# Performance work log

Hardware: AMD Instinct MI355X
Metric: run time of the kernel (lower is better)

Reference implementation:

```python
import jax, jax.numpy as jnp
import numpy as np

N_NODES = 512
IN_FEATURES = 512
N_HEADS = 8
N_HIDDEN = 64  # out_features // n_heads
NEG_SLOPE = 0.2


def setup_inputs() -> dict:
    key = jax.random.key(0)
    k_h, k_ws, k_wt, k_a, k_adj = jax.random.split(key, 5)
    lim_w = 1.0 / np.sqrt(IN_FEATURES)
    lim_a = 1.0 / np.sqrt(N_HIDDEN)
    h = jax.random.normal(k_h, (1, N_NODES, IN_FEATURES), dtype=jnp.float32)
    # nn.Linear weights: [out, in]
    W_source = jax.random.uniform(k_ws, (N_HEADS * N_HIDDEN, IN_FEATURES), jnp.float32, -lim_w, lim_w)
    W_target = jax.random.uniform(k_wt, (N_HEADS * N_HIDDEN, IN_FEATURES), jnp.float32, -lim_w, lim_w)
    attn_w = jax.random.uniform(k_a, (N_HIDDEN,), jnp.float32, -lim_a, lim_a)  # Linear(n_hidden, 1)
    adjacency_matrix = jax.random.randint(k_adj, (N_NODES, N_NODES, 1), 0, 2, dtype=jnp.int32)
    return {"h": h, "W_source": W_source, "W_target": W_target,
            "attn_w": attn_w, "adjacency_matrix": adjacency_matrix}


def reference(h, W_source, W_target, attn_w, adjacency_matrix):
    n_nodes = h.shape[1]
    x = h[0]  # [N, D]; module assumes batch == 1
    g_source = (x @ W_source.T).reshape(n_nodes, N_HEADS, N_HIDDEN)  # [N,H,F]
    g_target = (x @ W_target.T).reshape(n_nodes, N_HEADS, N_HIDDEN)  # [N,H,F]
    # g_sum[i, j] = g_source[j] + g_target[i]  (repeat / repeat_interleave semantics)
    g_sum = g_source[None, :, :, :] + g_target[:, None, :, :]  # [N,N,H,F]
    act = jnp.where(g_sum >= 0, g_sum, NEG_SLOPE * g_sum)       # LeakyReLU
    scores = jnp.einsum('ijhf,f->ijh', act, attn_w)              # [N,N,H]
    scores = jnp.where(adjacency_matrix == 0, -jnp.inf, scores)  # adj broadcasts over heads
    attention = jax.nn.softmax(scores, axis=1)                   # softmax over source nodes j
    # dropout p applied at eval -> identity
    head_output = jnp.einsum('ijh,jhf->ihf', attention, g_target)  # [N,H,F]
    out = head_output.reshape(n_nodes, N_HEADS * N_HIDDEN)         # is_concat=True
    return out, attention
```

## Files before the change

### kernel.cpp

```cpp
#include <hip/hip_runtime.h>
#include <hip/hip_bf16.h>

#define NN 512
#define IND 512
#define NH 8
#define NF 64
#define NEG_SLOPE 0.2f

__global__ __launch_bounds__(256) void gemm_xwT(
    const float* __restrict__ X,
    const float* __restrict__ Ws,
    const float* __restrict__ Wt,
    float* __restrict__ Gs, float* __restrict__ Gt)
{
    const float* W = (blockIdx.z == 0) ? Ws : Wt;
    float* C = (blockIdx.z == 0) ? Gs : Gt;

    __shared__ float As[32][33];
    __shared__ float Bs[32][33];

    const int tid = threadIdx.x;
    const int n0 = blockIdx.y * 32;
    const int o0 = blockIdx.x * 32;
    const int row = tid >> 3;
    const int kg  = (tid & 7) * 4;
    const int ty = tid >> 4;
    const int tx = tid & 15;

    float c00 = 0.f, c01 = 0.f, c10 = 0.f, c11 = 0.f;

    for (int kt = 0; kt < IND; kt += 32) {
        float4 pa = *reinterpret_cast<const float4*>(X + (size_t)(n0 + row) * IND + kt + kg);
        As[row][kg + 0] = pa.x;
        As[row][kg + 1] = pa.y;
        As[row][kg + 2] = pa.z;
        As[row][kg + 3] = pa.w;
        float4 pb = *reinterpret_cast<const float4*>(W + (size_t)(o0 + row) * IND + kt + kg);
        Bs[row][kg + 0] = pb.x;
        Bs[row][kg + 1] = pb.y;
        Bs[row][kg + 2] = pb.z;
        Bs[row][kg + 3] = pb.w;
        __syncthreads();
        #pragma unroll
        for (int k = 0; k < 32; ++k) {
            float a0 = As[ty][k], a1 = As[ty + 16][k];
            float b0 = Bs[tx][k], b1 = Bs[tx + 16][k];
            c00 += a0 * b0; c01 += a0 * b1;
            c10 += a1 * b0; c11 += a1 * b1;
        }
        __syncthreads();
    }
    C[(size_t)(n0 + ty) * IND + o0 + tx]            = c00;
    C[(size_t)(n0 + ty) * IND + o0 + tx + 16]       = c01;
    C[(size_t)(n0 + ty + 16) * IND + o0 + tx]       = c10;
    C[(size_t)(n0 + ty + 16) * IND + o0 + tx + 16]  = c11;
}

__global__ __launch_bounds__(256) void gat_attn(
    const float* __restrict__ Gs, const float* __restrict__ Gt,
    const float* __restrict__ attn_w,
    const int* __restrict__ adj,
    float* __restrict__ out_feat,
    float* __restrict__ out_att)
{
    __shared__ float s_gt[4][64];
    __shared__ float s_w[64];
    __shared__ float s_sc[4][512];
    __shared__ float s_red[4][4][64];

    const int tid = threadIdx.x;
    const int i0 = blockIdx.x * 4;
    const int h  = blockIdx.y;

    {
        int ii = tid >> 6, f = tid & 63;
        s_gt[ii][f] = Gt[(size_t)(i0 + ii) * IND + h * NF + f];
        if (tid < 64) s_w[tid] = attn_w[tid];
    }
    __syncthreads();

    #pragma unroll
    for (int rep = 0; rep < 2; ++rep) {
        int j = tid + rep * 256;
        float a0 = 0.f, a1 = 0.f, a2 = 0.f, a3 = 0.f;
        const float4* gp = reinterpret_cast<const float4*>(Gs + (size_t)j * IND + h * NF);
        #pragma unroll 4
        for (int f4 = 0; f4 < 16; ++f4) {
            float4 g = gp[f4];
            #pragma unroll
            for (int c = 0; c < 4; ++c) {
                float gv = (c == 0) ? g.x : (c == 1) ? g.y : (c == 2) ? g.z : g.w;
                int f = f4 * 4 + c;
                float w = s_w[f];
                float t;
                t = gv + s_gt[0][f]; t = (t >= 0.f) ? t : NEG_SLOPE * t; a0 += t * w;
                t = gv + s_gt[1][f]; t = (t >= 0.f) ? t : NEG_SLOPE * t; a1 += t * w;
                t = gv + s_gt[2][f]; t = (t >= 0.f) ? t : NEG_SLOPE * t; a2 += t * w;
                t = gv + s_gt[3][f]; t = (t >= 0.f) ? t : NEG_SLOPE * t; a3 += t * w;
            }
        }
        s_sc[0][j] = adj[(size_t)(i0 + 0) * NN + j] ? a0 : -INFINITY;
        s_sc[1][j] = adj[(size_t)(i0 + 1) * NN + j] ? a1 : -INFINITY;
        s_sc[2][j] = adj[(size_t)(i0 + 2) * NN + j] ? a2 : -INFINITY;
        s_sc[3][j] = adj[(size_t)(i0 + 3) * NN + j] ? a3 : -INFINITY;
    }
    __syncthreads();

    {
        const int wave = tid >> 6, lane = tid & 63;
        const int ii = wave;
        float m = -INFINITY;
        #pragma unroll
        for (int r = 0; r < 8; ++r) m = fmaxf(m, s_sc[ii][lane + r * 64]);
        #pragma unroll
        for (int off = 32; off >= 1; off >>= 1) m = fmaxf(m, __shfl_xor(m, off, 64));
        float e[8];
        float sum = 0.f;
        #pragma unroll
        for (int r = 0; r < 8; ++r) {
            float v = s_sc[ii][lane + r * 64];
            float ev = __expf(v - m);
            e[r] = ev;
            sum += ev;
        }
        #pragma unroll
        for (int off = 32; off >= 1; off >>= 1) sum += __shfl_xor(sum, off, 64);
        float inv = 1.f / sum;
        int i = i0 + ii;
        #pragma unroll
        for (int r = 0; r < 8; ++r) {
            int j = lane + r * 64;
            float a = e[r] * inv;
            s_sc[ii][j] = a;
            out_att[((size_t)i * NN + j) * NH + h] = a;
        }
    }
    __syncthreads();

    {
        const int f = tid & 63, q = tid >> 6;
        float a0 = 0.f, a1 = 0.f, a2 = 0.f, a3 = 0.f;
        for (int j = q * 128; j < q * 128 + 128; ++j) {
            float gv = Gt[(size_t)j * IND + h * NF + f];
            a0 += s_sc[0][j] * gv;
            a1 += s_sc[1][j] * gv;
            a2 += s_sc[2][j] * gv;
            a3 += s_sc[3][j] * gv;
        }
        s_red[q][0][f] = a0; s_red[q][1][f] = a1;
        s_red[q][2][f] = a2; s_red[q][3][f] = a3;
    }
    __syncthreads();
    {
        int ii = tid >> 6, f = tid & 63;
        float s = s_red[0][ii][f] + s_red[1][ii][f] + s_red[2][ii][f] + s_red[3][ii][f];
        out_feat[(size_t)(i0 + ii) * (NH * NF) + h * NF + f] = s;
    }
}

extern "C" void kernel_launch(void* const* d_in, const int* in_sizes, int n_in,
                              void* d_out, int out_size, void* d_ws, size_t ws_size,
                              hipStream_t stream) {
    const float* X  = (const float*)d_in[0];
    const float* Ws = (const float*)d_in[1];
    const float* Wt = (const float*)d_in[2];
    const float* aw = (const float*)d_in[3];
    const int* adj  = (const int*)d_in[4];

    float* Gs = (float*)d_ws;
    float* Gt = Gs + (size_t)NN * IND;

    float* out_feat = (float*)d_out;
    float* out_att  = out_feat + (size_t)NN * NH * NF;

    hipLaunchKernelGGL(gemm_xwT, dim3(16, 16, 2), dim3(256), 0, stream,
                       X, Ws, Wt, Gs, Gt);
    hipLaunchKernelGGL(gat_attn, dim3(NN / 4, NH), dim3(256), 0, stream,
                       Gs, Gt, aw, adj, out_feat, out_att);
}
```

Measured before the change: 120.9 us.

## Transpose inputs, compute Gs transposed via new GEMM, rework attention score loop

Adds a transpose kernel for X and W_target, then replaces the shared-memory tiled GEMM with a register-accumulating GEMM that splits K across waves. This GEMM writes Gs in a [feature, node] layout so the score loop reads contiguous float2 across nodes. LeakyReLU is rewritten as 0.6x+0.4|x| fused into FMAs, and the aggregation loop reads attention weights as float4 from shared memory. It adds an extra kernel launch and more workspace traffic for the transposes.

New measurement: 108.6 us. 1.11x faster.

```diff
diff --git a/kernel.cpp b/kernel.cpp
--- a/kernel.cpp
+++ b/kernel.cpp
@@ -1,114 +1,144 @@
 #include <hip/hip_runtime.h>
-#include <hip/hip_bf16.h>
 
 #define NN 512
 #define IND 512
 #define NH 8
 #define NF 64
-#define NEG_SLOPE 0.2f
-
-__global__ __launch_bounds__(256) void gemm_xwT(
-    const float* __restrict__ X,
-    const float* __restrict__ Ws,
-    const float* __restrict__ Wt,
-    float* __restrict__ Gs, float* __restrict__ Gt)
+
+__global__ __launch_bounds__(256) void transpose512(
+    const float* __restrict__ X, float* __restrict__ Xt,
+    const float* __restrict__ Wtg, float* __restrict__ Wtg_t)
 {
-    const float* W = (blockIdx.z == 0) ? Ws : Wt;
-    float* C = (blockIdx.z == 0) ? Gs : Gt;
-
-    __shared__ float As[32][33];
-    __shared__ float Bs[32][33];
-
+    const float* src = blockIdx.z ? Wtg : X;
+    float* dst       = blockIdx.z ? Wtg_t : Xt;
+    __shared__ float tile[32][33];
     const int tid = threadIdx.x;
-    const int n0 = blockIdx.y * 32;
-    const int o0 = blockIdx.x * 32;
-    const int row = tid >> 3;
-    const int kg  = (tid & 7) * 4;
-    const int ty = tid >> 4;
-    const int tx = tid & 15;
-
-    float c00 = 0.f, c01 = 0.f, c10 = 0.f, c11 = 0.f;
-
-    for (int kt = 0; kt < IND; kt += 32) {
-        float4 pa = *reinterpret_cast<const float4*>(X + (size_t)(n0 + row) * IND + kt + kg);
-        As[row][kg + 0] = pa.x;
-        As[row][kg + 1] = pa.y;
-        As[row][kg + 2] = pa.z;
-        As[row][kg + 3] = pa.w;
-        float4 pb = *reinterpret_cast<const float4*>(W + (size_t)(o0 + row) * IND + kt + kg);
-        Bs[row][kg + 0] = pb.x;
-        Bs[row][kg + 1] = pb.y;
-        Bs[row][kg + 2] = pb.z;
-        Bs[row][kg + 3] = pb.w;
-        __syncthreads();
-        #pragma unroll
-        for (int k = 0; k < 32; ++k) {
-            float a0 = As[ty][k], a1 = As[ty + 16][k];
-            float b0 = Bs[tx][k], b1 = Bs[tx + 16][k];
-            c00 += a0 * b0; c01 += a0 * b1;
-            c10 += a1 * b0; c11 += a1 * b1;
-        }
-        __syncthreads();
-    }
-    C[(size_t)(n0 + ty) * IND + o0 + tx]            = c00;
-    C[(size_t)(n0 + ty) * IND + o0 + tx + 16]       = c01;
-    C[(size_t)(n0 + ty + 16) * IND + o0 + tx]       = c10;
-    C[(size_t)(n0 + ty + 16) * IND + o0 + tx + 16]  = c11;
+    const int tx = tid & 31, ty4 = (tid >> 5) * 4;
+    const int x  = blockIdx.x * 32 + tx;
+    const int y0 = blockIdx.y * 32 + ty4;
+    #pragma unroll
+    for (int r = 0; r < 4; ++r)
+        tile[ty4 + r][tx] = src[(size_t)(y0 + r) * NN + x];
+    __syncthreads();
+    const int xo  = blockIdx.y * 32 + tx;
+    const int yo0 = blockIdx.x * 32 + ty4;
+    #pragma unroll
+    for (int r = 0; r < 4; ++r)
+        dst[(size_t)(yo0 + r) * NN + xo] = tile[tx][ty4 + r];
+}
+
+__global__ __launch_bounds__(256) void gemm_tn(
+    const float* __restrict__ Sa, const float* __restrict__ Va, float* __restrict__ Ca,
+    const float* __restrict__ Sb, const float* __restrict__ Vb, float* __restrict__ Cb)
+{
+    const float* S = blockIdx.z ? Sb : Sa;
+    const float* V = blockIdx.z ? Vb : Va;
+    float*       C = blockIdx.z ? Cb : Ca;
+
+    __shared__ float2 sp[2][4][64];
+
+    const int tid  = threadIdx.x;
+    const int wv   = __builtin_amdgcn_readfirstlane(tid >> 6);
+    const int lane = tid & 63;
+    const int rg = wv & 1, kh = wv >> 1;
+    const int r0 = blockIdx.y * 8 + rg * 4;
+    const int c0 = blockIdx.x * 128 + lane * 2;
+
+    const float* Sp = S + (size_t)r0 * IND + kh * 256;
+    const float* Vp = V + (size_t)kh * 256 * NN + c0;
+
+    float2 a0 = {0.f, 0.f}, a1 = {0.f, 0.f}, a2 = {0.f, 0.f}, a3 = {0.f, 0.f};
+    #pragma unroll 8
+    for (int k = 0; k < 256; ++k) {
+        float2 v = *reinterpret_cast<const float2*>(Vp + (size_t)k * NN);
+        float s0 = Sp[k];
+        float s1 = Sp[IND + k];
+        float s2 = Sp[2 * IND + k];
+        float s3 = Sp[3 * IND + k];
+        a0.x = fmaf(s0, v.x, a0.x); a0.y = fmaf(s0, v.y, a0.y);
+        a1.x = fmaf(s1, v.x, a1.x); a1.y = fmaf(s1, v.y, a1.y);
+        a2.x = fmaf(s2, v.x, a2.x); a2.y = fmaf(s2, v.y, a2.y);
+        a3.x = fmaf(s3, v.x, a3.x); a3.y = fmaf(s3, v.y, a3.y);
+    }
+    if (kh) {
+        sp[rg][0][lane] = a0; sp[rg][1][lane] = a1;
+        sp[rg][2][lane] = a2; sp[rg][3][lane] = a3;
+    }
+    __syncthreads();
+    if (!kh) {
+        float2 p;
+        p = sp[rg][0][lane]; a0.x += p.x; a0.y += p.y;
+        p = sp[rg][1][lane]; a1.x += p.x; a1.y += p.y;
+        p = sp[rg][2][lane]; a2.x += p.x; a2.y += p.y;
+        p = sp[rg][3][lane]; a3.x += p.x; a3.y += p.y;
+        *reinterpret_cast<float2*>(C + (size_t)(r0 + 0) * NN + c0) = a0;
+        *reinterpret_cast<float2*>(C + (size_t)(r0 + 1) * NN + c0) = a1;
+        *reinterpret_cast<float2*>(C + (size_t)(r0 + 2) * NN + c0) = a2;
+        *reinterpret_cast<float2*>(C + (size_t)(r0 + 3) * NN + c0) = a3;
+    }
 }
 
 __global__ __launch_bounds__(256) void gat_attn(
-    const float* __restrict__ Gs, const float* __restrict__ Gt,
+    const float* __restrict__ Gs_t,
+    const float* __restrict__ Gt,
     const float* __restrict__ attn_w,
-    const int* __restrict__ adj,
+    const int*   __restrict__ adj,
     float* __restrict__ out_feat,
     float* __restrict__ out_att)
 {
-    __shared__ float s_gt[4][64];
-    __shared__ float s_w[64];
     __shared__ float s_sc[4][512];
     __shared__ float s_red[4][4][64];
 
     const int tid = threadIdx.x;
-    const int i0 = blockIdx.x * 4;
-    const int h  = blockIdx.y;
-
-    {
-        int ii = tid >> 6, f = tid & 63;
-        s_gt[ii][f] = Gt[(size_t)(i0 + ii) * IND + h * NF + f];
-        if (tid < 64) s_w[tid] = attn_w[tid];
-    }
-    __syncthreads();
-
-    #pragma unroll
-    for (int rep = 0; rep < 2; ++rep) {
-        int j = tid + rep * 256;
-        float a0 = 0.f, a1 = 0.f, a2 = 0.f, a3 = 0.f;
-        const float4* gp = reinterpret_cast<const float4*>(Gs + (size_t)j * IND + h * NF);
+    const int i0  = blockIdx.x * 4;
+    const int h   = blockIdx.y;
+
+    {
+        const int jj = tid * 2;
+        float2 acc0 = {0.f,0.f}, acc1 = {0.f,0.f}, acc2 = {0.f,0.f}, acc3 = {0.f,0.f};
+        const float* gsp = Gs_t + (size_t)h * NF * NN + jj;
+        const float* gtp = Gt + (size_t)i0 * IND + h * NF;
         #pragma unroll 4
-        for (int f4 = 0; f4 < 16; ++f4) {
-            float4 g = gp[f4];
-            #pragma unroll
-            for (int c = 0; c < 4; ++c) {
-                float gv = (c == 0) ? g.x : (c == 1) ? g.y : (c == 2) ? g.z : g.w;
-                int f = f4 * 4 + c;
-                float w = s_w[f];
-                float t;
-                t = gv + s_gt[0][f]; t = (t >= 0.f) ? t : NEG_SLOPE * t; a0 += t * w;
-                t = gv + s_gt[1][f]; t = (t >= 0.f) ? t : NEG_SLOPE * t; a1 += t * w;
-                t = gv + s_gt[2][f]; t = (t >= 0.f) ? t : NEG_SLOPE * t; a2 += t * w;
-                t = gv + s_gt[3][f]; t = (t >= 0.f) ? t : NEG_SLOPE * t; a3 += t * w;
-            }
-        }
-        s_sc[0][j] = adj[(size_t)(i0 + 0) * NN + j] ? a0 : -INFINITY;
-        s_sc[1][j] = adj[(size_t)(i0 + 1) * NN + j] ? a1 : -INFINITY;
-        s_sc[2][j] = adj[(size_t)(i0 + 2) * NN + j] ? a2 : -INFINITY;
-        s_sc[3][j] = adj[(size_t)(i0 + 3) * NN + j] ? a3 : -INFINITY;
-    }
-    __syncthreads();
-
-    {
-        const int wave = tid >> 6, lane = tid & 63;
-        const int ii = wave;
+        for (int f = 0; f < NF; ++f) {
+            float w  = attn_w[f];
+            float w6 = 0.6f * w, w4 = 0.4f * w;
+            float2 g = *reinterpret_cast<const float2*>(gsp + (size_t)f * NN);
+            float gt0 = gtp[f];
+            float gt1 = gtp[IND + f];
+            float gt2 = gtp[2 * IND + f];
+            float gt3 = gtp[3 * IND + f];
+            float tx, ty;
+            tx = g.x + gt0; ty = g.y + gt0;
+            acc0.x = fmaf(w4, fabsf(tx), fmaf(w6, tx, acc0.x));
+            acc0.y = fmaf(w4, fabsf(ty), fmaf(w6, ty, acc0.y));
+            tx = g.x + gt1; ty = g.y + gt1;
+            acc1.x = fmaf(w4, fabsf(tx), fmaf(w6, tx, acc1.x));
+            acc1.y = fmaf(w4, fabsf(ty), fmaf(w6, ty, acc1.y));
+            tx = g.x + gt2; ty = g.y + gt2;
+            acc2.x = fmaf(w4, fabsf(tx), fmaf(w6, tx, acc2.x));
+            acc2.y = fmaf(w4, fabsf(ty), fmaf(w6, ty, acc2.y));
+            tx = g.x + gt3; ty = g.y + gt3;
+            acc3.x = fmaf(w4, fabsf(tx), fmaf(w6, tx, acc3.x));
+            acc3.y = fmaf(w4, fabsf(ty), fmaf(w6, ty, acc3.y));
+        }
+        int2 ad;
+        ad = *reinterpret_cast<const int2*>(adj + (size_t)(i0 + 0) * NN + jj);
+        s_sc[0][jj]     = ad.x ? acc0.x : -INFINITY;
+        s_sc[0][jj + 1] = ad.y ? acc0.y : -INFINITY;
+        ad = *reinterpret_cast<const int2*>(adj + (size_t)(i0 + 1) * NN + jj);
+        s_sc[1][jj]     = ad.x ? acc1.x : -INFINITY;
+        s_sc[1][jj + 1] = ad.y ? acc1.y : -INFINITY;
+        ad = *reinterpret_cast<const int2*>(adj + (size_t)(i0 + 2) * NN + jj);
+        s_sc[2][jj]     = ad.x ? acc2.x : -INFINITY;
+        s_sc[2][jj + 1] = ad.y ? acc2.y : -INFINITY;
+        ad = *reinterpret_cast<const int2*>(adj + (size_t)(i0 + 3) * NN + jj);
+        s_sc[3][jj]     = ad.x ? acc3.x : -INFINITY;
+        s_sc[3][jj + 1] = ad.y ? acc3.y : -INFINITY;
+    }
+    __syncthreads();
+
+    {
+        const int ii = tid >> 6, lane = tid & 63;
         float m = -INFINITY;
         #pragma unroll
         for (int r = 0; r < 8; ++r) m = fmaxf(m, s_sc[ii][lane + r * 64]);
@@ -118,15 +148,14 @@
         float sum = 0.f;
         #pragma unroll
         for (int r = 0; r < 8; ++r) {
-            float v = s_sc[ii][lane + r * 64];
-            float ev = __expf(v - m);
+            float ev = __expf(s_sc[ii][lane + r * 64] - m);
             e[r] = ev;
             sum += ev;
         }
         #pragma unroll
         for (int off = 32; off >= 1; off >>= 1) sum += __shfl_xor(sum, off, 64);
         float inv = 1.f / sum;
-        int i = i0 + ii;
+        const int i = i0 + ii;
         #pragma unroll
         for (int r = 0; r < 8; ++r) {
             int j = lane + r * 64;
@@ -138,21 +167,37 @@
     __syncthreads();
 
     {
-        const int f = tid & 63, q = tid >> 6;
-        float a0 = 0.f, a1 = 0.f, a2 = 0.f, a3 = 0.f;
-        for (int j = q * 128; j < q * 128 + 128; ++j) {
-            float gv = Gt[(size_t)j * IND + h * NF + f];
-            a0 += s_sc[0][j] * gv;
-            a1 += s_sc[1][j] * gv;
-            a2 += s_sc[2][j] * gv;
-            a3 += s_sc[3][j] * gv;
-        }
-        s_red[q][0][f] = a0; s_red[q][1][f] = a1;
-        s_red[q][2][f] = a2; s_red[q][3][f] = a3;
-    }
-    __syncthreads();
-    {
-        int ii = tid >> 6, f = tid & 63;
+        const int w = tid >> 6, lane = tid & 63;
+        const int jb = w * 128;
+        float o0 = 0.f, o1 = 0.f, o2 = 0.f, o3 = 0.f;
+        const float* gtc = Gt + h * NF + lane;
+        #pragma unroll 4
+        for (int s = 0; s < 32; ++s) {
+            const int j = jb + 4 * s;
+            float4 b0 = *reinterpret_cast<const float4*>(&s_sc[0][j]);
+            float4 b1 = *reinterpret_cast<const float4*>(&s_sc[1][j]);
+            float4 b2 = *reinterpret_cast<const float4*>(&s_sc[2][j]);
+            float4 b3 = *reinterpret_cast<const float4*>(&s_sc[3][j]);
+            float gv;
+            gv = gtc[(size_t)(j + 0) * IND];
+            o0 = fmaf(b0.x, gv, o0); o1 = fmaf(b1.x, gv, o1);
+            o2 = fmaf(b2.x, gv, o2); o3 = fmaf(b3.x, gv, o3);
+            gv = gtc[(size_t)(j + 1) * IND];
+            o0 = fmaf(b0.y, gv, o0); o1 = fmaf(b1.y, gv, o1);
+            o2 = fmaf(b2.y, gv, o2); o3 = fmaf(b3.y, gv, o3);
+            gv = gtc[(size_t)(j + 2) * IND];
+            o0 = fmaf(b0.z, gv, o0); o1 = fmaf(b1.z, gv, o1);
+            o2 = fmaf(b2.z, gv, o2); o3 = fmaf(b3.z, gv, o3);
+            gv = gtc[(size_t)(j + 3) * IND];
+            o0 = fmaf(b0.w, gv, o0); o1 = fmaf(b1.w, gv, o1);
+            o2 = fmaf(b2.w, gv, o2); o3 = fmaf(b3.w, gv, o3);
+        }
+        s_red[w][0][lane] = o0; s_red[w][1][lane] = o1;
+        s_red[w][2][lane] = o2; s_red[w][3][lane] = o3;
+    }
+    __syncthreads();
+    {
+        const int ii = tid >> 6, f = tid & 63;
         float s = s_red[0][ii][f] + s_red[1][ii][f] + s_red[2][ii][f] + s_red[3][ii][f];
         out_feat[(size_t)(i0 + ii) * (NH * NF) + h * NF + f] = s;
     }
@@ -161,20 +206,24 @@
 extern "C" void kernel_launch(void* const* d_in, const int* in_sizes, int n_in,
                               void* d_out, int out_size, void* d_ws, size_t ws_size,
                               hipStream_t stream) {
-    const float* X  = (const float*)d_in[0];
-    const float* Ws = (const float*)d_in[1];
-    const float* Wt = (const float*)d_in[2];
-    const float* aw = (const float*)d_in[3];
-    const int* adj  = (const int*)d_in[4];
-
-    float* Gs = (float*)d_ws;
-    float* Gt = Gs + (size_t)NN * IND;
+    const float* X   = (const float*)d_in[0];
+    const float* Ws  = (const float*)d_in[1];
+    const float* Wtg = (const float*)d_in[2];
+    const float* aw  = (const float*)d_in[3];
+    const int*   adj = (const int*)d_in[4];
+
+    float* Xt    = (float*)d_ws;
+    float* Wtg_t = Xt    + (size_t)NN * IND;
+    float* Gs_t  = Wtg_t + (size_t)NN * IND;
+    float* Gt    = Gs_t  + (size_t)NN * IND;
 
     float* out_feat = (float*)d_out;
     float* out_att  = out_feat + (size_t)NN * NH * NF;
 
-    hipLaunchKernelGGL(gemm_xwT, dim3(16, 16, 2), dim3(256), 0, stream,
-                       X, Ws, Wt, Gs, Gt);
+    hipLaunchKernelGGL(transpose512, dim3(16, 16, 2), dim3(256), 0, stream,
+                       X, Xt, Wtg, Wtg_t);
+    hipLaunchKernelGGL(gemm_tn, dim3(4, 64, 2), dim3(256), 0, stream,
+                       Ws, Xt, Gs_t, X, Wtg_t, Gt);
     hipLaunchKernelGGL(gat_attn, dim3(NN / 4, NH), dim3(256), 0, stream,
-                       Gs, Gt, aw, adj, out_feat, out_att);
-}
+                       Gs_t, Gt, aw, adj, out_feat, out_att);
+}
```
